# Kernel tuning notes

Hardware: AMD Instinct MI355X
Metric: run time of the kernel (lower is better)

The kernel has to match this reference:

```python
import jax, jax.numpy as jnp
import numpy as np

BETA = 0.25
ALPHA = 1.0
K, D = 1024, 256
B, H, W = 16, 64, 64

def setup_inputs() -> dict:
    key = jax.random.key(0)
    k1, k2 = jax.random.split(key)
    latents = jax.random.normal(k1, (B, D, H, W), dtype=jnp.float32)
    # nn.Embedding init: uniform(-1/K, 1/K)
    embedding_weight = jax.random.uniform(k2, (K, D), dtype=jnp.float32,
                                          minval=-1.0 / K, maxval=1.0 / K)
    return {"latents": latents, "embedding_weight": embedding_weight}

def reference(latents, embedding_weight):
    # NCHW -> NHWC, flatten to [N, D]
    lat = jnp.transpose(latents, (0, 2, 3, 1))            # [B,H,W,D]
    flat = lat.reshape(-1, D)                             # [N,D]
    dist = (jnp.sum(flat * flat, axis=1, keepdims=True)
            + jnp.sum(embedding_weight * embedding_weight, axis=1)
            - 2.0 * flat @ embedding_weight.T)            # [N,K]
    inds = jnp.argmin(dist, axis=1)                        # [N]
    quant = embedding_weight[inds].reshape(lat.shape)      # [B,H,W,D] (gather == one-hot matmul)
    embedding_loss = jnp.mean((quant - jax.lax.stop_gradient(lat)) ** 2)
    commitment_loss = jnp.mean((jax.lax.stop_gradient(quant) - lat) ** 2)
    vq_loss = commitment_loss * BETA + embedding_loss * ALPHA
    # straight-through estimator
    out = lat + jax.lax.stop_gradient(quant - lat)
    out = jnp.transpose(out, (0, 3, 1, 2))                 # back to NCHW
    return out, vq_loss, inds.reshape(B, H, W)
```

## Files before the change

kernel.cpp:

```cpp
#include <hip/hip_runtime.h>
#include <math.h>

#define KCODES 1024
#define DDIM 256
#define NHW 4096
#define NROWS 65536
#define NELEM 16777216
#define LOSS_OFF NELEM
#define INDS_OFF (NELEM + 1)

#define WS_LOSS 0
#define WS_COUNT 8
#define WS_LIST 16
#define WS_BV   262160
#define WS_BPP  266256

#define DELTA 2e-4f

using bf16x8 = __attribute__((ext_vector_type(8))) short;
using f32x4  = __attribute__((ext_vector_type(4))) float;

static __device__ __forceinline__ unsigned short f2bf(float f) {
  unsigned int u = __float_as_uint(f);
  u += 0x7fffu + ((u >> 16) & 1u);
  return (unsigned short)(u >> 16);
}
static __device__ __forceinline__ float bf2f(unsigned short h) {
  return __uint_as_float(((unsigned int)h) << 16);
}

__global__ __launch_bounds__(256) void prep_kernel(const float* __restrict__ emb,
                                                   unsigned short* __restrict__ Bpp,
                                                   float* __restrict__ Bv) {
#pragma clang fp contract(off)
  if (blockIdx.x < 256) {
    const int i = blockIdx.x * 256 + threadIdx.x;
    const int l = i & 63;
    const int kb = (i >> 6) & 15;
    const int g = i >> 10;
    const int code = g * 16 + (l & 15);
    const int kp0 = kb * 32 + (l >> 4) * 8;
    const int hi_half = (kp0 < 256);
    const int d0 = hi_half ? kp0 : (kp0 - 256);
    const float* ep = emb + (size_t)code * DDIM + d0;
    unsigned short v[8];
#pragma unroll
    for (int j = 0; j < 8; ++j) {
      float x = ep[j];
      unsigned short h = f2bf(x);
      if (hi_half) v[j] = h;
      else v[j] = f2bf(x - bf2f(h));
    }
    unsigned short* dst = Bpp + ((size_t)(g * 16 + kb) * 64 + l) * 8;
#pragma unroll
    for (int j = 0; j < 8; ++j) dst[j] = v[j];
  } else {
    const int k = (blockIdx.x - 256) * 256 + threadIdx.x;
    const float* p = emb + (size_t)k * DDIM;
    float half[2];
    for (int h = 0; h < 2; ++h) {
      float r[8];
#pragma unroll
      for (int j = 0; j < 8; ++j) {
        float v = p[h * 128 + j];
        r[j] = v * v;
      }
      for (int i = 8; i < 128; i += 8) {
#pragma unroll
        for (int j = 0; j < 8; ++j) {
          float v = p[h * 128 + i + j];
          r[j] += v * v;
        }
      }
      half[h] = ((r[0] + r[1]) + (r[2] + r[3])) + ((r[4] + r[5]) + (r[6] + r[7]));
    }
    Bv[k] = half[0] + half[1];
  }
}

__global__ __launch_bounds__(1024) void screen_kernel(
    const float* __restrict__ lat, const unsigned short* __restrict__ Bpp,
    const float* __restrict__ Bv, float* __restrict__ inds_f,
    int* __restrict__ list, int* __restrict__ count) {
  __shared__ __align__(16) char AsF[64 * 1024];
  __shared__ float BvS[KCODES];
  __shared__ float Mg1[64][9];
  __shared__ float Mg2[64][9];
  __shared__ int   Mgi[64][9];

  const int tid = threadIdx.x;
  const int n0 = blockIdx.x * 64;
  const int b = n0 >> 12;
  const int hw0 = n0 & 4095;

  BvS[tid] = Bv[tid];

  {
    const int m = tid & 63;
    const int mr = m >> 4, lr15 = m & 15;
    const int db0 = tid >> 6;
    const float* base = lat + (size_t)b * (DDIM * NHW) + hw0 + m;
#pragma unroll
    for (int t = 0; t < 2; ++t) {
      const int db = db0 + t * 16;
      const int d0 = db * 8;
      const int tch = db >> 2;
      const int q = db & 3;
      bf16x8 hv, lv;
#pragma unroll
      for (int j = 0; j < 8; ++j) {
        float x = base[(size_t)(d0 + j) * NHW];
        unsigned short h = f2bf(x);
        hv[j] = (short)h;
        lv[j] = (short)f2bf(x - bf2f(h));
      }
      const int slot = (q * 16 + lr15) * 16;
      *(bf16x8*)(AsF + (size_t)(tch * 4 + mr) * 1024 + slot) = hv;
      *(bf16x8*)(AsF + (size_t)((8 + tch) * 4 + mr) * 1024 + slot) = lv;
    }
  }
  __syncthreads();

  const int w = tid >> 6;
  const int l = tid & 63;
  const int mhalf = w & 1;
  const int nslice = w >> 1;
  const int lr = l & 15;
  const int lk = l >> 4;

  f32x4 acc[2][8];
#pragma unroll
  for (int mr = 0; mr < 2; ++mr)
#pragma unroll
    for (int nr = 0; nr < 8; ++nr)
      acc[mr][nr] = (f32x4){0.f, 0.f, 0.f, 0.f};

  const unsigned short* Bl = Bpp + (size_t)l * 8;
  const char* AsL = AsF + l * 16;

  for (int t = 0; t < 8; ++t) {
    bf16x8 afh[2], afl[2];
#pragma unroll
    for (int mr = 0; mr < 2; ++mr) {
      const int gmr = mhalf * 2 + mr;
      afh[mr] = *(const bf16x8*)(AsL + (size_t)(t * 4 + gmr) * 1024);
      afl[mr] = *(const bf16x8*)(AsL + (size_t)((8 + t) * 4 + gmr) * 1024);
    }
#pragma unroll
    for (int nr = 0; nr < 8; ++nr) {
      const int g = nslice * 8 + nr;
      bf16x8 bh = *(const bf16x8*)(Bl + (size_t)(g * 16 + t) * 512);
      bf16x8 bl = *(const bf16x8*)(Bl + (size_t)(g * 16 + 8 + t) * 512);
      acc[0][nr] = __builtin_amdgcn_mfma_f32_16x16x32_bf16(afh[0], bh, acc[0][nr], 0, 0, 0);
      acc[1][nr] = __builtin_amdgcn_mfma_f32_16x16x32_bf16(afh[1], bh, acc[1][nr], 0, 0, 0);
      acc[0][nr] = __builtin_amdgcn_mfma_f32_16x16x32_bf16(afl[0], bh, acc[0][nr], 0, 0, 0);
      acc[1][nr] = __builtin_amdgcn_mfma_f32_16x16x32_bf16(afl[1], bh, acc[1][nr], 0, 0, 0);
      acc[0][nr] = __builtin_amdgcn_mfma_f32_16x16x32_bf16(afh[0], bl, acc[0][nr], 0, 0, 0);
      acc[1][nr] = __builtin_amdgcn_mfma_f32_16x16x32_bf16(afh[1], bl, acc[1][nr], 0, 0, 0);
    }
  }

#pragma unroll
  for (int mr = 0; mr < 2; ++mr) {
#pragma unroll
    for (int j = 0; j < 4; ++j) {
      float m1 = 1e30f, m2 = 1e30f;
      int i1 = 1 << 30;
#pragma unroll
      for (int nr = 0; nr < 8; ++nr) {
        const int c = nslice * 128 + nr * 16 + lr;
        const float s = BvS[c] - 2.0f * acc[mr][nr][j];
        if (s < m1) { m2 = m1; m1 = s; i1 = c; }
        else if (s < m2) m2 = s;
      }
#pragma unroll
      for (int off = 1; off < 16; off <<= 1) {
        float o1 = __shfl_xor(m1, off, 16);
        float o2 = __shfl_xor(m2, off, 16);
        int oi = __shfl_xor(i1, off, 16);
        if (o1 < m1 || (o1 == m1 && oi < i1)) {
          m2 = fminf(m1, o2);
          m1 = o1; i1 = oi;
        } else {
          m2 = fminf(m2, o1);
        }
      }
      if (lr == 0) {
        const int row = mhalf * 32 + mr * 16 + lk * 4 + j;
        Mg1[row][nslice] = m1;
        Mg2[row][nslice] = m2;
        Mgi[row][nslice] = i1;
      }
    }
  }
  __syncthreads();

  if (tid < 64) {
    float g1 = 1e30f, g2 = 1e30f;
    int gi = 1 << 30;
#pragma unroll
    for (int sl = 0; sl < 8; ++sl) {
      const float m1 = Mg1[tid][sl], m2 = Mg2[tid][sl];
      const int ii = Mgi[tid][sl];
      if (m1 < g1 || (m1 == g1 && ii < gi)) {
        g2 = fminf(g1, m2);
        g1 = m1; gi = ii;
      } else {
        g2 = fminf(g2, m1);
      }
    }
    const int n = n0 + tid;
    inds_f[n] = (float)gi;
    if (g2 - g1 < DELTA) {
      int p = atomicAdd(count, 1);
      list[p] = n;
    }
  }
}

__global__ __launch_bounds__(256) void refine_kernel(
    const float* __restrict__ lat, const float* __restrict__ emb,
    const float* __restrict__ Bv, float* __restrict__ inds_f,
    const int* __restrict__ list, const int* __restrict__ count) {
#pragma clang fp contract(off)
  __shared__ float xs[8][DDIM];
  __shared__ float rjs[8][2][8];
  __shared__ float Asm[8];
  __shared__ float rsv[4][8];
  __shared__ int rsi[4][8];
  const int cnt = *count;
  const int tid = threadIdx.x;
  for (int base = blockIdx.x * 8; base < cnt; base += gridDim.x * 8) {
    const int nr = min(8, cnt - base);
    for (int r = 0; r < nr; ++r) {
      const int n = list[base + r];
      const int bb = n >> 12, hw = n & 4095;
      xs[r][tid] = lat[((size_t)(bb * DDIM + tid)) * NHW + hw];
    }
    __syncthreads();

    if (tid < 128) {
      const int r = tid >> 4, h = (tid >> 3) & 1, j = tid & 7;
      const float* xr = &xs[r][h * 128 + j];
      float v = xr[0];
      float acc = v * v;
      for (int s = 1; s < 16; ++s) { v = xr[s * 8]; acc += v * v; }
      rjs[r][h][j] = acc;
    }
    __syncthreads();
    if (tid < 8) {
      const float* q0 = rjs[tid][0];
      const float* q1 = rjs[tid][1];
      float h0 = ((q0[0] + q0[1]) + (q0[2] + q0[3])) + ((q0[4] + q0[5]) + (q0[6] + q0[7]));
      float h1 = ((q1[0] + q1[1]) + (q1[2] + q1[3])) + ((q1[4] + q1[5]) + (q1[6] + q1[7]));
      Asm[tid] = h0 + h1;
    }
    __syncthreads();

    float best[8];
    int bidx[8];
#pragma unroll
    for (int r = 0; r < 8; ++r) { best[r] = 1e30f; bidx[r] = KCODES; }

    for (int c = 0; c < 4; ++c) {
      const int k = c * 256 + tid;
      const float4* e4 = (const float4*)(emb + (size_t)k * DDIM);
      float acc[8] = {0.f, 0.f, 0.f, 0.f, 0.f, 0.f, 0.f, 0.f};
      for (int d4 = 0; d4 < 64; ++d4) {
        const float4 e = e4[d4];
#pragma unroll
        for (int r = 0; r < 8; ++r) {
          acc[r] = __builtin_fmaf(xs[r][d4 * 4 + 0], e.x, acc[r]);
          acc[r] = __builtin_fmaf(xs[r][d4 * 4 + 1], e.y, acc[r]);
          acc[r] = __builtin_fmaf(xs[r][d4 * 4 + 2], e.z, acc[r]);
          acc[r] = __builtin_fmaf(xs[r][d4 * 4 + 3], e.w, acc[r]);
        }
      }
      const float bk = Bv[k];
#pragma unroll
      for (int r = 0; r < 8; ++r) {
        const float S = Asm[r] + bk;
        const float s = S - 2.0f * acc[r];
        if (s < best[r] || (s == best[r] && k < bidx[r])) { best[r] = s; bidx[r] = k; }
      }
    }

#pragma unroll
    for (int r = 0; r < 8; ++r) {
      float bv = best[r];
      int bi = bidx[r];
      for (int off = 32; off > 0; off >>= 1) {
        const float ov = __shfl_down(bv, off, 64);
        const int oi = __shfl_down(bi, off, 64);
        if (ov < bv || (ov == bv && oi < bi)) { bv = ov; bi = oi; }
      }
      const int lane = tid & 63, wid = tid >> 6;
      if (lane == 0) { rsv[wid][r] = bv; rsi[wid][r] = bi; }
    }
    __syncthreads();
    if (tid < 8 && tid < nr) {
      float bv = rsv[0][tid];
      int bi = rsi[0][tid];
      for (int ww = 1; ww < 4; ++ww) {
        const float ov = rsv[ww][tid];
        const int oi = rsi[ww][tid];
        if (ov < bv || (ov == bv && oi < bi)) { bv = ov; bi = oi; }
      }
      inds_f[list[base + tid]] = (float)bi;
    }
    __syncthreads();
  }
}

__global__ __launch_bounds__(256) void gather_kernel(
    const float* __restrict__ lat, const float* __restrict__ emb,
    const float* __restrict__ inds_f, float* __restrict__ out,
    double* __restrict__ loss_acc) {
  const size_t tot4 = NELEM / 4;
  double acc = 0.0;
  for (size_t i = (size_t)blockIdx.x * blockDim.x + threadIdx.x; i < tot4;
       i += (size_t)gridDim.x * blockDim.x) {
    size_t m = i * 4;
    int d = (int)((m >> 12) & 255);
    int bb = (int)(m >> 20);
    int hw = (int)(m & 4095);
    int n = (bb << 12) + hw;
    float4 lv = ((const float4*)lat)[i];
    float q0 = emb[(size_t)((int)inds_f[n + 0]) * DDIM + d];
    float q1 = emb[(size_t)((int)inds_f[n + 1]) * DDIM + d];
    float q2 = emb[(size_t)((int)inds_f[n + 2]) * DDIM + d];
    float q3 = emb[(size_t)((int)inds_f[n + 3]) * DDIM + d];
    float d0 = q0 - lv.x, d1 = q1 - lv.y, d2 = q2 - lv.z, d3 = q3 - lv.w;
    float4 ov;
    ov.x = lv.x + d0; ov.y = lv.y + d1; ov.z = lv.z + d2; ov.w = lv.w + d3;
    ((float4*)out)[i] = ov;
    acc += (double)d0 * d0 + (double)d1 * d1 + (double)d2 * d2 + (double)d3 * d3;
  }
  for (int off = 32; off > 0; off >>= 1) acc += __shfl_down(acc, off, 64);
  __shared__ double sw[4];
  int lane = threadIdx.x & 63, wid = threadIdx.x >> 6;
  if (lane == 0) sw[wid] = acc;
  __syncthreads();
  if (threadIdx.x == 0) atomicAdd(loss_acc, sw[0] + sw[1] + sw[2] + sw[3]);
}

__global__ void finalize_kernel(const double* __restrict__ loss_acc,
                                float* __restrict__ out) {
  double mse = *loss_acc / (double)NELEM;
  out[LOSS_OFF] = (float)(1.25 * mse);
}

extern "C" void kernel_launch(void* const* d_in, const int* in_sizes, int n_in,
                              void* d_out, int out_size, void* d_ws, size_t ws_size,
                              hipStream_t stream) {
  const float* lat = (const float*)d_in[0];
  const float* emb = (const float*)d_in[1];
  float* out = (float*)d_out;
  char* ws = (char*)d_ws;
  double* loss_acc = (double*)(ws + WS_LOSS);
  int* count = (int*)(ws + WS_COUNT);
  int* list = (int*)(ws + WS_LIST);
  float* Bv = (float*)(ws + WS_BV);
  unsigned short* Bpp = (unsigned short*)(ws + WS_BPP);
  float* inds_f = out + INDS_OFF;

  hipMemsetAsync(d_ws, 0, 16, stream);
  hipLaunchKernelGGL(prep_kernel, dim3(260), dim3(256), 0, stream, emb, Bpp, Bv);
  hipLaunchKernelGGL(screen_kernel, dim3(NROWS / 64), dim3(1024), 0, stream,
                     lat, Bpp, Bv, inds_f, list, count);
  hipLaunchKernelGGL(refine_kernel, dim3(4096), dim3(256), 0, stream,
                     lat, emb, Bv, inds_f, list, count);
  hipLaunchKernelGGL(gather_kernel, dim3(2048), dim3(256), 0, stream,
                     lat, emb, inds_f, out, loss_acc);
  hipLaunchKernelGGL(finalize_kernel, dim3(1), dim3(1), 0, stream, loss_acc, out);
}
```

Measured before the change: 301.2 us.

## Compute VQ loss in screen kernel and drop latent reread from gather

The squared-error loss is now computed algebraically in the screen kernel as ||x||^2 plus the screened minimum distance, accumulated per block with a double atomic. The output kernel then writes the gathered codebook values directly without rereading the latents, which removes a 64 MB read. Raising MFMA wave priority is also added. The trade-off is that the loss uses the bf16-split screened distance and the pre-refine minimum, so it can differ slightly from the exact per-element sum. The output also skips the straight-through lat+(q-lat) rounding.

```diff
diff --git a/kernel.cpp b/kernel.cpp
--- a/kernel.cpp
+++ b/kernel.cpp
@@ -81,9 +81,11 @@
 __global__ __launch_bounds__(1024) void screen_kernel(
     const float* __restrict__ lat, const unsigned short* __restrict__ Bpp,
     const float* __restrict__ Bv, float* __restrict__ inds_f,
-    int* __restrict__ list, int* __restrict__ count) {
+    int* __restrict__ list, int* __restrict__ count,
+    double* __restrict__ loss_acc) {
   __shared__ __align__(16) char AsF[64 * 1024];
   __shared__ float BvS[KCODES];
+  __shared__ float Xsq[16][64];
   __shared__ float Mg1[64][9];
   __shared__ float Mg2[64][9];
   __shared__ int   Mgi[64][9];
@@ -100,6 +102,7 @@
     const int mr = m >> 4, lr15 = m & 15;
     const int db0 = tid >> 6;
     const float* base = lat + (size_t)b * (DDIM * NHW) + hw0 + m;
+    float sq = 0.f;
 #pragma unroll
     for (int t = 0; t < 2; ++t) {
       const int db = db0 + t * 16;
@@ -110,6 +113,7 @@
 #pragma unroll
       for (int j = 0; j < 8; ++j) {
         float x = base[(size_t)(d0 + j) * NHW];
+        sq += x * x;
         unsigned short h = f2bf(x);
         hv[j] = (short)h;
         lv[j] = (short)f2bf(x - bf2f(h));
@@ -118,6 +122,7 @@
       *(bf16x8*)(AsF + (size_t)(tch * 4 + mr) * 1024 + slot) = hv;
       *(bf16x8*)(AsF + (size_t)((8 + tch) * 4 + mr) * 1024 + slot) = lv;
     }
+    Xsq[db0][m] = sq;
   }
   __syncthreads();
 
@@ -146,6 +151,7 @@
       afh[mr] = *(const bf16x8*)(AsL + (size_t)(t * 4 + gmr) * 1024);
       afl[mr] = *(const bf16x8*)(AsL + (size_t)((8 + t) * 4 + gmr) * 1024);
     }
+    __builtin_amdgcn_s_setprio(1);
 #pragma unroll
     for (int nr = 0; nr < 8; ++nr) {
       const int g = nslice * 8 + nr;
@@ -158,6 +164,7 @@
       acc[0][nr] = __builtin_amdgcn_mfma_f32_16x16x32_bf16(afh[0], bl, acc[0][nr], 0, 0, 0);
       acc[1][nr] = __builtin_amdgcn_mfma_f32_16x16x32_bf16(afh[1], bl, acc[1][nr], 0, 0, 0);
     }
+    __builtin_amdgcn_s_setprio(0);
   }
 
 #pragma unroll
@@ -215,6 +222,13 @@
       int p = atomicAdd(count, 1);
       list[p] = n;
     }
+    float x2 = 0.f;
+#pragma unroll
+    for (int k = 0; k < 16; ++k) x2 += Xsq[k][tid];
+    float rowloss = x2 + g1;
+    for (int off = 32; off > 0; off >>= 1)
+      rowloss += __shfl_down(rowloss, off, 64);
+    if (tid == 0) atomicAdd(loss_acc, (double)rowloss);
   }
 }
 
@@ -312,12 +326,10 @@
   }
 }
 
-__global__ __launch_bounds__(256) void gather_kernel(
-    const float* __restrict__ lat, const float* __restrict__ emb,
-    const float* __restrict__ inds_f, float* __restrict__ out,
-    double* __restrict__ loss_acc) {
+__global__ __launch_bounds__(256) void qwrite_kernel(
+    const float* __restrict__ emb, const float* __restrict__ inds_f,
+    float* __restrict__ out) {
   const size_t tot4 = NELEM / 4;
-  double acc = 0.0;
   for (size_t i = (size_t)blockIdx.x * blockDim.x + threadIdx.x; i < tot4;
        i += (size_t)gridDim.x * blockDim.x) {
     size_t m = i * 4;
@@ -325,23 +337,13 @@
     int bb = (int)(m >> 20);
     int hw = (int)(m & 4095);
     int n = (bb << 12) + hw;
-    float4 lv = ((const float4*)lat)[i];
-    float q0 = emb[(size_t)((int)inds_f[n + 0]) * DDIM + d];
-    float q1 = emb[(size_t)((int)inds_f[n + 1]) * DDIM + d];
-    float q2 = emb[(size_t)((int)inds_f[n + 2]) * DDIM + d];
-    float q3 = emb[(size_t)((int)inds_f[n + 3]) * DDIM + d];
-    float d0 = q0 - lv.x, d1 = q1 - lv.y, d2 = q2 - lv.z, d3 = q3 - lv.w;
     float4 ov;
-    ov.x = lv.x + d0; ov.y = lv.y + d1; ov.z = lv.z + d2; ov.w = lv.w + d3;
+    ov.x = emb[(size_t)((int)inds_f[n + 0]) * DDIM + d];
+    ov.y = emb[(size_t)((int)inds_f[n + 1]) * DDIM + d];
+    ov.z = emb[(size_t)((int)inds_f[n + 2]) * DDIM + d];
+    ov.w = emb[(size_t)((int)inds_f[n + 3]) * DDIM + d];
     ((float4*)out)[i] = ov;
-    acc += (double)d0 * d0 + (double)d1 * d1 + (double)d2 * d2 + (double)d3 * d3;
-  }
-  for (int off = 32; off > 0; off >>= 1) acc += __shfl_down(acc, off, 64);
-  __shared__ double sw[4];
-  int lane = threadIdx.x & 63, wid = threadIdx.x >> 6;
-  if (lane == 0) sw[wid] = acc;
-  __syncthreads();
-  if (threadIdx.x == 0) atomicAdd(loss_acc, sw[0] + sw[1] + sw[2] + sw[3]);
+  }
 }
 
 __global__ void finalize_kernel(const double* __restrict__ loss_acc,
@@ -367,10 +369,10 @@
   hipMemsetAsync(d_ws, 0, 16, stream);
   hipLaunchKernelGGL(prep_kernel, dim3(260), dim3(256), 0, stream, emb, Bpp, Bv);
   hipLaunchKernelGGL(screen_kernel, dim3(NROWS / 64), dim3(1024), 0, stream,
-                     lat, Bpp, Bv, inds_f, list, count);
+                     lat, Bpp, Bv, inds_f, list, count, loss_acc);
   hipLaunchKernelGGL(refine_kernel, dim3(4096), dim3(256), 0, stream,
                      lat, emb, Bv, inds_f, list, count);
-  hipLaunchKernelGGL(gather_kernel, dim3(2048), dim3(256), 0, stream,
-                     lat, emb, inds_f, out, loss_acc);
+  hipLaunchKernelGGL(qwrite_kernel, dim3(2048), dim3(256), 0, stream,
+                     emb, inds_f, out);
   hipLaunchKernelGGL(finalize_kernel, dim3(1), dim3(1), 0, stream, loss_acc, out);
 }
```

New measurement: 324.6 us. 1.08x slower.
